# Kernel tuning notes

Hardware: AMD Instinct MI355X
Metric: run time of the kernel (lower is better)

## Reference

```python
import jax, jax.numpy as jnp
import numpy as np

B, S, H = 2, 2048, 2048
NH, HD = 32, 64            # num heads, head dim (H = NH*HD)
FFN = 8192
EPS = 1e-5


def _layernorm(x, g, b):
    mu = jnp.mean(x, axis=-1, keepdims=True)
    var = jnp.mean(jnp.square(x - mu), axis=-1, keepdims=True)
    return (x - mu) * jax.lax.rsqrt(var + EPS) * g + b


def setup_inputs() -> dict:
    key = jax.random.key(0)
    ks = jax.random.split(key, 8)
    s = lambda fan_in: 1.0 / np.sqrt(fan_in)
    return {
        "x": jax.random.normal(ks[0], (B, S, H), dtype=jnp.float32),
        "ln1_g": jnp.ones((H,), jnp.float32),
        "ln1_b": jnp.zeros((H,), jnp.float32),
        "w_qkv": jax.random.normal(ks[1], (H, 3 * H), jnp.float32) * s(H),
        "b_qkv": jnp.zeros((3 * H,), jnp.float32),
        "w_proj": jax.random.normal(ks[2], (H, H), jnp.float32) * s(H),
        "b_proj": jnp.zeros((H,), jnp.float32),
        "ln2_g": jnp.ones((H,), jnp.float32),
        "ln2_b": jnp.zeros((H,), jnp.float32),
        "w1": jax.random.normal(ks[3], (H, FFN), jnp.float32) * s(H),
        "b1": jnp.zeros((FFN,), jnp.float32),
        "w2": jax.random.normal(ks[4], (FFN, H), jnp.float32) * s(FFN),
        "b2": jnp.zeros((H,), jnp.float32),
    }


def reference(x, ln1_g, ln1_b, w_qkv, b_qkv, w_proj, b_proj,
              ln2_g, ln2_b, w1, b1, w2, b2):
    # Pre-LN attention block (dropout in eval mode -> identity)
    res = x
    h = _layernorm(x, ln1_g, ln1_b)
    qkv = h @ w_qkv + b_qkv                       # [B,S,3H]
    qkv = qkv.reshape(B, S, NH, 3 * HD)           # matches tf reshape+split on axis 3
    q, k, v = jnp.split(qkv, 3, axis=3)           # each [B,S,NH,HD]
    scores = jnp.einsum('bqhd,bkhd->bhqk', q, k) / jnp.sqrt(jnp.float32(HD))
    probs = jax.nn.softmax(scores, axis=-1)       # [B,NH,S,S]
    ctx = jnp.einsum('bhqk,bkhd->bqhd', probs, v).reshape(B, S, H)
    x = ctx @ w_proj + b_proj
    x = res + x
    # Pre-LN MLP block
    res = x
    h = _layernorm(x, ln2_g, ln2_b)
    h = jax.nn.gelu(h @ w1 + b1, approximate=True)
    h = h @ w2 + b2
    return h + res
```

## Files before the change

### kernel.cpp

```cpp
#include <hip/hip_runtime.h>
#include <hip/hip_bf16.h>
#include <math.h>


typedef __attribute__((ext_vector_type(8))) short bf16x8;
typedef __attribute__((ext_vector_type(4))) float f32x4;
typedef __attribute__((ext_vector_type(16))) float f32x16;

#define DEV __device__ __forceinline__

static constexpr int SEQ  = 2048;
static constexpr int HID  = 2048;
static constexpr int NHEAD = 32;
static constexpr int HDIM = 64;
static constexpr int NFFN = 8192;
static constexpr int NTOK = 2 * SEQ;
static constexpr int QKVW = 3 * HID;

#define QSCALE 0.1803368801111204f

#if defined(__has_builtin)
#if __has_builtin(__builtin_amdgcn_exp2f)
#define EXP2(x) __builtin_amdgcn_exp2f(x)
#endif
#endif
#ifndef EXP2
#define EXP2(x) exp2f(x)
#endif

#define VMCNT(n) asm volatile("s_waitcnt vmcnt(" #n ")" ::: "memory")
#define SB0()    __builtin_amdgcn_sched_barrier(0)

DEV ushort f2bf(float f) {
  unsigned u = __float_as_uint(f);
  return (ushort)((u + 0x7fffu + ((u >> 16) & 1u)) >> 16);
}

DEV void gload16(const void* g, void* l) {
  __builtin_amdgcn_global_load_lds(
      (const __attribute__((address_space(1))) unsigned int*)g,
      (__attribute__((address_space(3))) unsigned int*)l, 16, 0, 0);
}

__global__ __launch_bounds__(256) void tcvt_kernel(const float* __restrict__ in,
                                                   ushort* __restrict__ out,
                                                   int R, int C) {
  __shared__ ushort tile[64][72];
  const int tr = blockIdx.y * 64, tc = blockIdx.x * 64;
  const int t = threadIdx.x;
  const int rr = t >> 2, c4 = (t & 3) * 16;
  const float4* ip = (const float4*)(in + (size_t)(tr + rr) * C + tc + c4);
  float4 a0 = ip[0], a1 = ip[1], a2 = ip[2], a3 = ip[3];
  ushort* tp = &tile[rr][c4];
  tp[0]=f2bf(a0.x); tp[1]=f2bf(a0.y); tp[2]=f2bf(a0.z); tp[3]=f2bf(a0.w);
  tp[4]=f2bf(a1.x); tp[5]=f2bf(a1.y); tp[6]=f2bf(a1.z); tp[7]=f2bf(a1.w);
  tp[8]=f2bf(a2.x); tp[9]=f2bf(a2.y); tp[10]=f2bf(a2.z); tp[11]=f2bf(a2.w);
  tp[12]=f2bf(a3.x); tp[13]=f2bf(a3.y); tp[14]=f2bf(a3.z); tp[15]=f2bf(a3.w);
  __syncthreads();
  union { ushort u[8]; bf16x8 v; } p0, p1;
#pragma unroll
  for (int j = 0; j < 8; ++j) { p0.u[j] = tile[c4 + j][rr]; p1.u[j] = tile[c4 + 8 + j][rr]; }
  ushort* op = out + (size_t)(tc + rr) * R + tr + c4;
  *(bf16x8*)op = p0.v;
  *(bf16x8*)(op + 8) = p1.v;
}

__global__ __launch_bounds__(256) void ln_kernel(const float* __restrict__ x,
                                                 const float* __restrict__ g,
                                                 const float* __restrict__ bb,
                                                 ushort* __restrict__ out) {
  const int row = blockIdx.x, t = threadIdx.x;
  const float4* xv = (const float4*)(x + (size_t)row * HID);
  float4 a0 = xv[t * 2], a1 = xv[t * 2 + 1];
  float s  = a0.x + a0.y + a0.z + a0.w + a1.x + a1.y + a1.z + a1.w;
  float ss = a0.x*a0.x + a0.y*a0.y + a0.z*a0.z + a0.w*a0.w
           + a1.x*a1.x + a1.y*a1.y + a1.z*a1.z + a1.w*a1.w;
#pragma unroll
  for (int o = 32; o > 0; o >>= 1) { s += __shfl_down(s, o); ss += __shfl_down(ss, o); }
  __shared__ float red[8];
  const int w = t >> 6, l = t & 63;
  if (l == 0) { red[w] = s; red[4 + w] = ss; }
  __syncthreads();
  s  = red[0] + red[1] + red[2] + red[3];
  ss = red[4] + red[5] + red[6] + red[7];
  const float mu = s * (1.f / HID);
  const float rs = rsqrtf(ss * (1.f / HID) - mu * mu + 1e-5f);
  const float4* gv = (const float4*)g;
  const float4* bv = (const float4*)bb;
  float4 g0 = gv[t * 2], g1 = gv[t * 2 + 1], b0 = bv[t * 2], b1 = bv[t * 2 + 1];
  union { ushort u[8]; bf16x8 v; } p;
  p.u[0] = f2bf((a0.x - mu) * rs * g0.x + b0.x);
  p.u[1] = f2bf((a0.y - mu) * rs * g0.y + b0.y);
  p.u[2] = f2bf((a0.z - mu) * rs * g0.z + b0.z);
  p.u[3] = f2bf((a0.w - mu) * rs * g0.w + b0.w);
  p.u[4] = f2bf((a1.x - mu) * rs * g1.x + b1.x);
  p.u[5] = f2bf((a1.y - mu) * rs * g1.y + b1.y);
  p.u[6] = f2bf((a1.z - mu) * rs * g1.z + b1.z);
  p.u[7] = f2bf((a1.w - mu) * rs * g1.w + b1.w);
  *(bf16x8*)(out + (size_t)row * HID + t * 8) = p.v;
}

DEV void qkv_store(int row, int col, float v,
                   ushort* __restrict__ qpk, ushort* __restrict__ kpk,
                   ushort* __restrict__ vpk) {
  const int h = col / 192;
  const int c = col - h * 192;
  const int bh2 = (row >> 11) * 32 + h;
  const int t32 = (row >> 5) & 63;
  const int r5 = row & 31;
  if (c < 64) {
    const int s = c >> 4, hi2 = (c >> 3) & 1, j = c & 7;
    qpk[(((size_t)bh2 * 64 + t32) * 4 + s) * 512 + (hi2 * 32 + r5) * 8 + j] = f2bf(v * QSCALE);
  } else if (c < 128) {
    const int d = c - 64;
    const int s = d >> 4, hi2 = (d >> 3) & 1, j = d & 7;
    kpk[(((size_t)bh2 * 64 + t32) * 4 + s) * 512 + (hi2 * 32 + r5) * 8 + j] = f2bf(v);
  } else {
    const int d = c - 128;
    const int ks = r5 >> 4, hi2 = (r5 >> 3) & 1, j = r5 & 7;
    const int half = d >> 5, dl = d & 31;
    vpk[((((size_t)bh2 * 64 + t32) * 2 + ks) * 2 + half) * 512 + (hi2 * 32 + dl) * 8 + j] = f2bf(v);
  }
}

template <int BM, int EPI>
__global__ __launch_bounds__(512, 2) void gemm8p_kernel(
    const ushort* __restrict__ A, const ushort* __restrict__ BT,
    const float* __restrict__ bias, const float* __restrict__ res,
    void* __restrict__ outv,
    ushort* __restrict__ qpk, ushort* __restrict__ kpk, ushort* __restrict__ vpk,
    int M, int N, int K) {
  constexpr int MR = BM / 32;
  constexpr int MH = BM / 64;

  __shared__ ushort lds[2 * (BM * 64 + 256 * 64)];
  char* const a0p = (char*)lds;
  char* const b0p = a0p + BM * 128;
  char* const a1p = b0p + 32768;
  char* const b1p = a1p + BM * 128;

  const int t = threadIdx.x;
  const int w = t >> 6, l = t & 63;
  const int l16 = l & 15, lg = l >> 4;
  const int lr = l >> 3, lsl = l & 7;
  const int wm = w >> 2, wn = w & 3;
  const int l7 = l & 7;

  const int nwg = gridDim.x * gridDim.y;
  const int lin = blockIdx.y * gridDim.x + blockIdx.x;
  const int work = (lin & 7) * (nwg >> 3) + (lin >> 3);
  const int bn = work % gridDim.x, bm = work / gridDim.x;
  const int tm = bm * BM, tn = bn * 256;

  const int xk0 = (lg ^ l7) << 4;
  const int xk1 = ((lg + 4) ^ l7) << 4;
  const int aoff = (wm * (BM / 2) + l16) * 128;
  const int boff = (wn * 64 + l16) * 128;
  const char* rA0k0 = a0p + aoff + xk0;  const char* rA0k1 = a0p + aoff + xk1;
  const char* rA1k0 = a1p + aoff + xk0;  const char* rA1k1 = a1p + aoff + xk1;
  const char* rB0k0 = b0p + boff + xk0;  const char* rB0k1 = b0p + boff + xk1;
  const char* rB1k0 = b1p + boff + xk0;  const char* rB1k1 = b1p + boff + xk1;

  int rA00, rA01, rA10, rA11;
  if (BM == 256) {
    rA00 = 0 * 128 + 0 * 64 + w * 8 + lr;  rA01 = 1 * 128 + 0 * 64 + w * 8 + lr;
    rA10 = 0 * 128 + 1 * 64 + w * 8 + lr;  rA11 = 1 * 128 + 1 * 64 + w * 8 + lr;
  } else {
    const int ri = w * 8 + lr;
    rA00 = (ri >> 5) * 64 + 0 * 32 + (ri & 31);
    rA10 = (ri >> 5) * 64 + 1 * 32 + (ri & 31);
    rA01 = rA00; rA11 = rA10;
  }
  const int riB0 = w * 8 + lr, riB1 = 64 + w * 8 + lr;
  const int rB00 = (riB0 >> 5) * 64 + (riB0 & 31);
  const int rB01 = (riB1 >> 5) * 64 + (riB1 & 31);
  const int rB10 = (riB0 >> 5) * 64 + 32 + (riB0 & 31);
  const int rB11 = (riB1 >> 5) * 64 + 32 + (riB1 & 31);
  const int gcol = (lsl ^ lr) << 3;
  const ushort* pa00 = A + (size_t)(tm + rA00) * K + gcol;
  const ushort* pa01 = A + (size_t)(tm + rA01) * K + gcol;
  const ushort* pa10 = A + (size_t)(tm + rA10) * K + gcol;
  const ushort* pa11 = A + (size_t)(tm + rA11) * K + gcol;
  const ushort* pb00 = BT + (size_t)(tn + rB00) * K + gcol;
  const ushort* pb01 = BT + (size_t)(tn + rB01) * K + gcol;
  const ushort* pb10 = BT + (size_t)(tn + rB10) * K + gcol;
  const ushort* pb11 = BT + (size_t)(tn + rB11) * K + gcol;
  const int da00 = rA00 * 128 + lsl * 16, da01 = rA01 * 128 + lsl * 16;
  const int da10 = rA10 * 128 + lsl * 16, da11 = rA11 * 128 + lsl * 16;
  const int db00 = rB00 * 128 + lsl * 16, db01 = rB01 * 128 + lsl * 16;
  const int db10 = rB10 * 128 + lsl * 16, db11 = rB11 * 128 + lsl * 16;

  const f32x4 z4 = {0.f, 0.f, 0.f, 0.f};
  f32x4 acc[MR][4];
#pragma unroll
  for (int i = 0; i < MR; ++i)
#pragma unroll
    for (int j = 0; j < 4; ++j) acc[i][j] = z4;

  auto ktile = [&](const char* rAk0, const char* rAk1,
                   const char* rBk0, const char* rBk1,
                   char* NA, char* NB, int ktn, bool dost) {
    bf16x8 af[MH][2], bfr[2][2];
#pragma unroll
    for (int q = 0; q < 4; ++q) {
      const int mh = q >> 1, nh = q & 1;
      if ((q & 1) == 0) {
#pragma unroll
        for (int mi = 0; mi < MH; ++mi) {
          af[mi][0] = *(const bf16x8*)(rAk0 + mh * (BM / 4) * 128 + mi * 2048);
          af[mi][1] = *(const bf16x8*)(rAk1 + mh * (BM / 4) * 128 + mi * 2048);
        }
      }
#pragma unroll
      for (int ni = 0; ni < 2; ++ni) {
        bfr[ni][0] = *(const bf16x8*)(rBk0 + nh * 4096 + ni * 2048);
        bfr[ni][1] = *(const bf16x8*)(rBk1 + nh * 4096 + ni * 2048);
      }
      if (dost && q < 2) {
        if (q == 0) {
          gload16(pa00 + ktn, NA + da00);
          if (BM == 256) gload16(pa01 + ktn, NA + da01);
          gload16(pb00 + ktn, NB + db00);
          gload16(pb01 + ktn, NB + db01);
        } else {
          gload16(pa10 + ktn, NA + da10);
          if (BM == 256) gload16(pa11 + ktn, NA + da11);
          gload16(pb10 + ktn, NB + db10);
          gload16(pb11 + ktn, NB + db11);
        }
      }
      if (q == 0) {
        if (dost) { if (BM == 256) VMCNT(4); else VMCNT(3); }
        else VMCNT(0);
      }
      if (q == 3 && dost) { if (BM == 256) VMCNT(4); else VMCNT(3); }
      __builtin_amdgcn_s_barrier();
      asm volatile("s_waitcnt lgkmcnt(0)" ::: "memory");
      SB0();
      __builtin_amdgcn_s_setprio(1);
#pragma unroll
      for (int mi = 0; mi < MH; ++mi)
#pragma unroll
        for (int ni = 0; ni < 2; ++ni)
#pragma unroll
          for (int ks = 0; ks < 2; ++ks)
            acc[mh * MH + mi][nh * 2 + ni] = __builtin_amdgcn_mfma_f32_16x16x32_bf16(
                af[mi][ks], bfr[ni][ks], acc[mh * MH + mi][nh * 2 + ni], 0, 0, 0);
      __builtin_amdgcn_s_setprio(0);
    }
  };

  gload16(pa00, a0p + da00);
  if (BM == 256) gload16(pa01, a0p + da01);
  gload16(pb00, b0p + db00);
  gload16(pb01, b0p + db01);
  gload16(pa10, a0p + da10);
  if (BM == 256) gload16(pa11, a0p + da11);
  gload16(pb10, b0p + db10);
  gload16(pb11, b0p + db11);
  VMCNT(0);
  __builtin_amdgcn_s_barrier();

  const int nt = K >> 6;
  for (int it = 0; it < nt; it += 2) {
    ktile(rA0k0, rA0k1, rB0k0, rB0k1, a1p, b1p, (it + 1) << 6, true);
    ktile(rA1k0, rA1k1, rB1k0, rB1k1, a0p, b0p, (it + 2) << 6, (it + 2) < nt);
  }

  const int row0 = tm + wm * (BM / 2) + lg * 4;
  const int col0 = tn + wn * 64 + l16;
#pragma unroll
  for (int ni = 0; ni < 4; ++ni) {
    const int col = col0 + ni * 16;
    const float bvl = bias[col];
#pragma unroll
    for (int mi = 0; mi < MR; ++mi) {
#pragma unroll
      for (int r = 0; r < 4; ++r) {
        const int row = row0 + mi * 16 + r;
        float v = acc[mi][ni][r] + bvl;
        if (EPI == 1) {
          const size_t off = (size_t)row * N + col;
          ((float*)outv)[off] = v + res[off];
        } else if (EPI == 2) {
          const float u = 0.7978845608f * (v + 0.044715f * v * v * v);
          ((ushort*)outv)[(size_t)row * N + col] = f2bf(v / (1.f + __expf(-2.f * u)));
        } else if (EPI == 3) {
          qkv_store(row, col, v, qpk, kpk, vpk);
        } else {
          ((ushort*)outv)[(size_t)row * N + col] = f2bf(v);
        }
      }
    }
  }
}

__global__ __launch_bounds__(256) void attn_kernel(const ushort* __restrict__ qpk,
                                                   const ushort* __restrict__ kpk,
                                                   const ushort* __restrict__ vpk,
                                                   ushort* __restrict__ ctx) {
  const int lin = blockIdx.x + blockIdx.y * gridDim.x;
  const int work = (lin & 7) * 128 + (lin >> 3);
  const int qt = work & 15, bh = work >> 4;
  const int b = bh >> 5, h = bh & 31;
  const int t = threadIdx.x, w = t >> 6, l = t & 63;
  const int l32 = l & 31, hi = l >> 5;

  const ushort* qb = qpk + ((((size_t)bh * 64 + qt * 4 + w) * 4) * 64 + l) * 8;
  bf16x8 qf0 = *(const bf16x8*)(qb);
  bf16x8 qf1 = *(const bf16x8*)(qb + 512);
  bf16x8 qf2 = *(const bf16x8*)(qb + 1024);
  bf16x8 qf3 = *(const bf16x8*)(qb + 1536);

  const ushort* kbase = kpk + (size_t)bh * 131072 + l * 8;
  const ushort* vbase = vpk + (size_t)bh * 131072 + l * 8;

  f32x16 oacc0, oacc1;
#pragma unroll
  for (int r = 0; r < 16; ++r) { oacc0[r] = 0.f; oacc1[r] = 0.f; }
  float m = -1e30f, lsum = 0.f;
  const f32x16 z16 = {};

#define LOADK(k0, k1, k2, k3, kt) {                                           \
    const ushort* p_ = kbase + (size_t)(kt) * 2048;                           \
    k0 = *(const bf16x8*)(p_);        k1 = *(const bf16x8*)(p_ + 512);        \
    k2 = *(const bf16x8*)(p_ + 1024); k3 = *(const bf16x8*)(p_ + 1536); }
#define LOADV(v0, v1, v2, v3, kt) {                                           \
    const ushort* p_ = vbase + (size_t)(kt) * 2048;                           \
    v0 = *(const bf16x8*)(p_);        v1 = *(const bf16x8*)(p_ + 512);        \
    v2 = *(const bf16x8*)(p_ + 1024); v3 = *(const bf16x8*)(p_ + 1536); }

#define STEP(k0, k1, k2, k3, v0, v1, v2, v3) {                                \
    f32x16 s = __builtin_amdgcn_mfma_f32_32x32x16_bf16(k0, qf0, z16, 0, 0, 0);\
    s = __builtin_amdgcn_mfma_f32_32x32x16_bf16(k1, qf1, s, 0, 0, 0);         \
    s = __builtin_amdgcn_mfma_f32_32x32x16_bf16(k2, qf2, s, 0, 0, 0);         \
    s = __builtin_amdgcn_mfma_f32_32x32x16_bf16(k3, qf3, s, 0, 0, 0);         \
    float tm_ = s[0];                                                         \
    _Pragma("unroll") for (int r = 1; r < 16; ++r) tm_ = fmaxf(tm_, s[r]);    \
    tm_ = fmaxf(tm_, __shfl_xor(tm_, 32));                                    \
    if (!__all(tm_ - m <= 8.f)) {                                             \
      const float mn = fmaxf(m, tm_);                                         \
      const float sf = EXP2(m - mn);                                          \
      m = mn;                                                                 \
      lsum *= sf;                                                             \
      _Pragma("unroll") for (int r = 0; r < 16; ++r) {                        \
        const float f = __shfl(sf, (r & 3) + 8 * (r >> 2) + 4 * hi);          \
        oacc0[r] *= f; oacc1[r] *= f;                                         \
      }                                                                       \
    }                                                                         \
    float p[16];                                                              \
    _Pragma("unroll") for (int r = 0; r < 16; ++r) p[r] = EXP2(s[r] - m);     \
    float ls = 0.f;                                                           \
    _Pragma("unroll") for (int r = 0; r < 16; ++r) ls += p[r];                \
    lsum += ls;                                                               \
    unsigned pw[8];                                                           \
    _Pragma("unroll") for (int i = 0; i < 8; ++i)                             \
      asm("v_cvt_pk_bf16_f32 %0, %1, %2" : "=v"(pw[i]) : "v"(p[2*i]), "v"(p[2*i+1])); \
    unsigned a0 = pw[0], b0 = pw[2];                                          \
    asm("v_permlane32_swap_b32 %0, %1" : "+v"(a0), "+v"(b0));                 \
    unsigned a1 = pw[1], b1 = pw[3];                                          \
    asm("v_permlane32_swap_b32 %0, %1" : "+v"(a1), "+v"(b1));                 \
    unsigned a2 = pw[4], b2 = pw[6];                                          \
    asm("v_permlane32_swap_b32 %0, %1" : "+v"(a2), "+v"(b2));                 \
    unsigned a3 = pw[5], b3 = pw[7];                                          \
    asm("v_permlane32_swap_b32 %0, %1" : "+v"(a3), "+v"(b3));                 \
    union { unsigned uw[4]; bf16x8 v; } pa0, pa1;                             \
    pa0.uw[0] = a0; pa0.uw[1] = a1; pa0.uw[2] = b0; pa0.uw[3] = b1;           \
    pa1.uw[0] = a2; pa1.uw[1] = a3; pa1.uw[2] = b2; pa1.uw[3] = b3;           \
    oacc0 = __builtin_amdgcn_mfma_f32_32x32x16_bf16(pa0.v, v0, oacc0, 0, 0, 0);\
    oacc1 = __builtin_amdgcn_mfma_f32_32x32x16_bf16(pa0.v, v1, oacc1, 0, 0, 0);\
    oacc0 = __builtin_amdgcn_mfma_f32_32x32x16_bf16(pa1.v, v2, oacc0, 0, 0, 0);\
    oacc1 = __builtin_amdgcn_mfma_f32_32x32x16_bf16(pa1.v, v3, oacc1, 0, 0, 0);}

  bf16x8 ka0, ka1, ka2, ka3, kc0, kc1, kc2, kc3;
  LOADK(ka0, ka1, ka2, ka3, 0);
  for (int kt = 0; kt < 64; kt += 2) {
    bf16x8 va0, va1, va2, va3;
    LOADV(va0, va1, va2, va3, kt);
    LOADK(kc0, kc1, kc2, kc3, kt + 1);
    STEP(ka0, ka1, ka2, ka3, va0, va1, va2, va3);
    LOADV(va0, va1, va2, va3, kt + 1);
    if (kt + 2 < 64) LOADK(ka0, ka1, ka2, ka3, kt + 2);
    STEP(kc0, kc1, kc2, kc3, va0, va1, va2, va3);
  }
#undef LOADK
#undef LOADV
#undef STEP

  const float lf = lsum + __shfl_xor(lsum, 32);
  const float linv = 1.f / lf;
#pragma unroll
  for (int r = 0; r < 16; ++r) {
    const int qr = (r & 3) + 8 * (r >> 2);
    const float fac = __shfl(linv, qr + 4 * hi);
    const int row = qt * 128 + w * 32 + qr + 4 * hi;
    const size_t base = ((size_t)(b * SEQ + row)) * HID + h * 64 + l32;
    ctx[base]      = f2bf(oacc0[r] * fac);
    ctx[base + 32] = f2bf(oacc1[r] * fac);
  }
}

extern "C" void kernel_launch(void* const* d_in, const int* in_sizes, int n_in,
                              void* d_out, int out_size, void* d_ws, size_t ws_size,
                              hipStream_t stream) {
  const float* x      = (const float*)d_in[0];
  const float* ln1g   = (const float*)d_in[1];
  const float* ln1b   = (const float*)d_in[2];
  const float* w_qkv  = (const float*)d_in[3];
  const float* b_qkv  = (const float*)d_in[4];
  const float* w_proj = (const float*)d_in[5];
  const float* b_proj = (const float*)d_in[6];
  const float* ln2g   = (const float*)d_in[7];
  const float* ln2b   = (const float*)d_in[8];
  const float* w1     = (const float*)d_in[9];
  const float* b1     = (const float*)d_in[10];
  const float* w2     = (const float*)d_in[11];
  const float* b2     = (const float*)d_in[12];

  char* ws = (char*)d_ws;
  ushort* wqkvT  = (ushort*)(ws + 0);
  ushort* wprojT = (ushort*)(ws + 25165824);
  ushort* w1T    = (ushort*)(ws + 33554432);
  ushort* w2T    = (ushort*)(ws + 67108864);
  ushort* hbuf   = (ushort*)(ws + 100663296);
  ushort* qpk    = (ushort*)(ws + 117440512);
  ushort* kpk    = (ushort*)(ws + 134217728);
  ushort* vpk    = (ushort*)(ws + 150994944);
  ushort* ctxb   = (ushort*)(ws + 167772160);
  ushort* gelu   = (ushort*)(ws + 117440512);
  float*  x2     = (float*)(ws + 184549376);

  tcvt_kernel<<<dim3(96, 32),  256, 0, stream>>>(w_qkv,  wqkvT, 2048, 6144);
  tcvt_kernel<<<dim3(32, 32),  256, 0, stream>>>(w_proj, wprojT, 2048, 2048);
  tcvt_kernel<<<dim3(128, 32), 256, 0, stream>>>(w1,     w1T,   2048, 8192);
  tcvt_kernel<<<dim3(32, 128), 256, 0, stream>>>(w2,     w2T,   8192, 2048);

  ln_kernel<<<NTOK, 256, 0, stream>>>(x, ln1g, ln1b, hbuf);
  gemm8p_kernel<128, 3><<<dim3(24, 32), 512, 0, stream>>>(
      hbuf, wqkvT, b_qkv, nullptr, nullptr, qpk, kpk, vpk, NTOK, QKVW, HID);
  attn_kernel<<<dim3(16, 2 * NHEAD), 256, 0, stream>>>(qpk, kpk, vpk, ctxb);
  gemm8p_kernel<128, 1><<<dim3(8, 32), 512, 0, stream>>>(
      ctxb, wprojT, b_proj, x, x2, nullptr, nullptr, nullptr, NTOK, HID, HID);
  ln_kernel<<<NTOK, 256, 0, stream>>>(x2, ln2g, ln2b, hbuf);
  gemm8p_kernel<256, 2><<<dim3(32, 16), 512, 0, stream>>>(
      hbuf, w1T, b1, nullptr, gelu, nullptr, nullptr, nullptr, NTOK, NFFN, HID);
  gemm8p_kernel<128, 1><<<dim3(8, 32), 512, 0, stream>>>(
      gelu, w2T, b2, x2, (float*)d_out, nullptr, nullptr, nullptr, NTOK, HID, NFFN);
}
```

Baseline: 633.4 us.

## Add ping-pong pipelined 256x256 GEMM kernel for the FFN up-projection

Adds a new 256x256-tile bf16 GEMM kernel that splits each tile into four 128-wide halves in LDS. It interleaves per-half global-to-LDS loads with MFMA sub-blocks using barriers, explicit waitcnts and setprio, and uses an XOR-swizzled layout. It replaces the previous gemm8p<256,2> launch for the w1 GEMM with fused GELU, aiming to overlap memory traffic with matrix math more tightly. The many barriers and the 128KB LDS footprint cost occupancy and scheduling flexibility, in exchange for deeper software pipelining.

```diff
diff --git a/kernel.cpp b/kernel.cpp
--- a/kernel.cpp
+++ b/kernel.cpp
@@ -287,6 +287,176 @@
           ((ushort*)outv)[(size_t)row * N + col] = f2bf(v / (1.f + __expf(-2.f * u)));
         } else if (EPI == 3) {
           qkv_store(row, col, v, qpk, kpk, vpk);
+        } else {
+          ((ushort*)outv)[(size_t)row * N + col] = f2bf(v);
+        }
+      }
+    }
+  }
+}
+
+template <int EPI>
+__global__ __launch_bounds__(512, 2) void gemm256p_kernel(
+    const ushort* __restrict__ A, const ushort* __restrict__ BT,
+    const float* __restrict__ bias, const float* __restrict__ res,
+    void* __restrict__ outv, int M, int N, int K) {
+  __shared__ ushort lds[65536];
+  char* const L = (char*)lds;
+
+  const int t = threadIdx.x;
+  const int w = t >> 6, l = t & 63;
+  const int l16 = l & 15, lg = l >> 4, lr = l >> 3, lsl = l & 7, l7 = l & 7;
+  const int wm = w >> 2, wn = w & 3;
+
+  const int nwg = gridDim.x * gridDim.y;
+  const int lin = blockIdx.y * gridDim.x + blockIdx.x;
+  const int work = (lin & 7) * (nwg >> 3) + (lin >> 3);
+  const int bn = work % gridDim.x, bm = work / gridDim.x;
+  const int tm = bm * 256, tn = bn * 256;
+
+  char* Ab[2][2]; char* Bb[2][2];
+#pragma unroll
+  for (int par = 0; par < 2; ++par)
+#pragma unroll
+    for (int h = 0; h < 2; ++h) {
+      Ab[par][h] = L + (par * 2 + h) * 16384;
+      Bb[par][h] = L + 65536 + (par * 2 + h) * 16384;
+    }
+
+  const int xk0 = (lg ^ l7) << 4, xk1 = ((4 + lg) ^ l7) << 4;
+  const char* pA[2][2]; const char* pB[2][2];
+#pragma unroll
+  for (int par = 0; par < 2; ++par) {
+    const char* ab = Ab[par][wm] + l16 * 128;
+    const char* bb = Bb[par][wn >> 1] + ((wn & 1) * 64 + l16) * 128;
+    pA[par][0] = ab + xk0; pA[par][1] = ab + xk1;
+    pB[par][0] = bb + xk0; pB[par][1] = bb + xk1;
+  }
+
+  const int gcol = (lsl ^ lr) << 3;
+  const ushort* gA[2][2]; const ushort* gB[2][2];
+  int dst[2];
+#pragma unroll
+  for (int s = 0; s < 2; ++s) {
+    const int r = s * 64 + w * 8 + lr;
+    dst[s] = r * 128 + lsl * 16;
+#pragma unroll
+    for (int h = 0; h < 2; ++h) {
+      gA[h][s] = A + (size_t)(tm + h * 128 + r) * K + gcol;
+      gB[h][s] = BT + (size_t)(tn + h * 128 + r) * K + gcol;
+    }
+  }
+
+  f32x4 acc[8][4];
+  const f32x4 z4 = {0.f, 0.f, 0.f, 0.f};
+#pragma unroll
+  for (int i = 0; i < 8; ++i)
+#pragma unroll
+    for (int j = 0; j < 4; ++j) acc[i][j] = z4;
+
+  auto rdA = [&](int par, int mh, bf16x8 (&af)[4][2]) {
+#pragma unroll
+    for (int mi = 0; mi < 4; ++mi) {
+      af[mi][0] = *(const bf16x8*)(pA[par][0] + mh * 8192 + mi * 2048);
+      af[mi][1] = *(const bf16x8*)(pA[par][1] + mh * 8192 + mi * 2048);
+    }
+  };
+  auto rdB = [&](int par, int nh, bf16x8 (&bf)[2][2]) {
+#pragma unroll
+    for (int ni = 0; ni < 2; ++ni) {
+      bf[ni][0] = *(const bf16x8*)(pB[par][0] + nh * 4096 + ni * 2048);
+      bf[ni][1] = *(const bf16x8*)(pB[par][1] + nh * 4096 + ni * 2048);
+    }
+  };
+  auto mf16 = [&](int mh, int nh, bf16x8 (&af)[4][2], bf16x8 (&bf)[2][2]) {
+    __builtin_amdgcn_s_setprio(1);
+#pragma unroll
+    for (int mi = 0; mi < 4; ++mi)
+#pragma unroll
+      for (int ni = 0; ni < 2; ++ni)
+#pragma unroll
+        for (int ks = 0; ks < 2; ++ks)
+          acc[mh * 4 + mi][nh * 2 + ni] = __builtin_amdgcn_mfma_f32_16x16x32_bf16(
+              af[mi][ks], bf[ni][ks], acc[mh * 4 + mi][nh * 2 + ni], 0, 0, 0);
+    __builtin_amdgcn_s_setprio(0);
+  };
+#define BAR() __builtin_amdgcn_s_barrier()
+#define LGKM0() do { asm volatile("s_waitcnt lgkmcnt(0)" ::: "memory"); SB0(); } while (0)
+
+#pragma unroll
+  for (int h = 0; h < 2; ++h)
+#pragma unroll
+    for (int s = 0; s < 2; ++s) gload16(gA[h][s], Ab[0][h] + dst[s]);
+#pragma unroll
+  for (int h = 0; h < 2; ++h)
+#pragma unroll
+    for (int s = 0; s < 2; ++s) gload16(gB[h][s], Bb[0][h] + dst[s]);
+#pragma unroll
+  for (int h = 0; h < 2; ++h)
+#pragma unroll
+    for (int s = 0; s < 2; ++s) gload16(gB[h][s] + 64, Bb[1][h] + dst[s]);
+  VMCNT(4);
+  BAR();
+
+  const int nt = K >> 6;
+  for (int it = 0; it < nt; it += 2) {
+    const int k1 = (it + 1) << 6, k2 = (it + 2) << 6, k3 = (it + 3) << 6;
+    const bool s2 = (it + 2) < nt;
+    bf16x8 af[4][2], b0[2][2], b1[2][2];
+    rdA(0, 0, af); rdB(0, 0, b0);
+    gload16(gA[0][0] + k1, Ab[1][0] + dst[0]);
+    gload16(gA[0][1] + k1, Ab[1][0] + dst[1]);
+    BAR(); LGKM0(); mf16(0, 0, af, b0); BAR();
+    rdB(0, 1, b1);
+    gload16(gA[1][0] + k1, Ab[1][1] + dst[0]);
+    gload16(gA[1][1] + k1, Ab[1][1] + dst[1]);
+    BAR(); LGKM0(); mf16(0, 1, af, b1); BAR();
+    rdA(0, 1, af);
+    if (s2) { gload16(gB[0][0] + k2, Bb[0][0] + dst[0]);
+              gload16(gB[0][1] + k2, Bb[0][0] + dst[1]); }
+    BAR(); LGKM0(); mf16(1, 1, af, b1); BAR();
+    if (s2) { gload16(gB[1][0] + k2, Bb[0][1] + dst[0]);
+              gload16(gB[1][1] + k2, Bb[0][1] + dst[1]); }
+    BAR(); LGKM0(); mf16(1, 0, af, b0);
+    if (s2) VMCNT(4); else VMCNT(0);
+    BAR();
+    rdA(1, 0, af); rdB(1, 0, b0);
+    if (s2) { gload16(gA[0][0] + k2, Ab[0][0] + dst[0]);
+              gload16(gA[0][1] + k2, Ab[0][0] + dst[1]); }
+    BAR(); LGKM0(); mf16(0, 0, af, b0); BAR();
+    rdB(1, 1, b1);
+    if (s2) { gload16(gA[1][0] + k2, Ab[0][1] + dst[0]);
+              gload16(gA[1][1] + k2, Ab[0][1] + dst[1]); }
+    BAR(); LGKM0(); mf16(0, 1, af, b1); BAR();
+    rdA(1, 1, af);
+    if (s2) { gload16(gB[0][0] + k3, Bb[1][0] + dst[0]);
+              gload16(gB[0][1] + k3, Bb[1][0] + dst[1]); }
+    BAR(); LGKM0(); mf16(1, 1, af, b1); BAR();
+    if (s2) { gload16(gB[1][0] + k3, Bb[1][1] + dst[0]);
+              gload16(gB[1][1] + k3, Bb[1][1] + dst[1]); }
+    BAR(); LGKM0(); mf16(1, 0, af, b0);
+    if (s2) VMCNT(4); else VMCNT(0);
+    BAR();
+  }
+#undef BAR
+#undef LGKM0
+
+#pragma unroll
+  for (int nf = 0; nf < 4; ++nf) {
+    const int col = tn + wn * 64 + nf * 16 + l16;
+    const float bvl = bias[col];
+#pragma unroll
+    for (int mf = 0; mf < 8; ++mf) {
+#pragma unroll
+      for (int r = 0; r < 4; ++r) {
+        const int row = tm + wm * 128 + mf * 16 + lg * 4 + r;
+        float v = acc[mf][nf][r] + bvl;
+        if (EPI == 1) {
+          const size_t off = (size_t)row * N + col;
+          ((float*)outv)[off] = v + res[off];
+        } else if (EPI == 2) {
+          const float u = 0.7978845608f * (v + 0.044715f * v * v * v);
+          ((ushort*)outv)[(size_t)row * N + col] = f2bf(v / (1.f + __expf(-2.f * u)));
         } else {
           ((ushort*)outv)[(size_t)row * N + col] = f2bf(v);
         }
@@ -442,8 +612,8 @@
   gemm8p_kernel<128, 1><<<dim3(8, 32), 512, 0, stream>>>(
       ctxb, wprojT, b_proj, x, x2, nullptr, nullptr, nullptr, NTOK, HID, HID);
   ln_kernel<<<NTOK, 256, 0, stream>>>(x2, ln2g, ln2b, hbuf);
-  gemm8p_kernel<256, 2><<<dim3(32, 16), 512, 0, stream>>>(
-      hbuf, w1T, b1, nullptr, gelu, nullptr, nullptr, nullptr, NTOK, NFFN, HID);
+  gemm256p_kernel<2><<<dim3(32, 16), 512, 0, stream>>>(
+      hbuf, w1T, b1, nullptr, gelu, NTOK, NFFN, HID);
   gemm8p_kernel<128, 1><<<dim3(8, 32), 512, 0, stream>>>(
       gelu, w2T, b2, x2, (float*)d_out, nullptr, nullptr, nullptr, NTOK, HID, NFFN);
 }
```

Result: slower. 1.001 ms (+58.1%).

## Add triple-buffered 128x256 GEMM kernel with XCD-aware tile swizzle

Applied to the files above, without the earlier changes.

Introduces a new GEMM kernel, gemm3b, that keeps three LDS stages so global loads run two K-tiles ahead of the MFMA work. It remaps workgroup IDs so neighbouring tiles are grouped across the 8 dispatch partitions, and raises wave priority around the MFMA block. The QKV, output-projection and FFN-down GEMMs switch to this kernel to hide memory latency better than the previous double-buffered one. In exchange it uses more LDS per block (about 144KB), which may limit occupancy, and it adds a sizeable macro-based code path.

```diff
diff --git a/kernel.cpp b/kernel.cpp
--- a/kernel.cpp
+++ b/kernel.cpp
@@ -275,6 +275,143 @@
     const float bvl = bias[col];
 #pragma unroll
     for (int mi = 0; mi < MR; ++mi) {
+#pragma unroll
+      for (int r = 0; r < 4; ++r) {
+        const int row = row0 + mi * 16 + r;
+        float v = acc[mi][ni][r] + bvl;
+        if (EPI == 1) {
+          const size_t off = (size_t)row * N + col;
+          ((float*)outv)[off] = v + res[off];
+        } else if (EPI == 2) {
+          const float u = 0.7978845608f * (v + 0.044715f * v * v * v);
+          ((ushort*)outv)[(size_t)row * N + col] = f2bf(v / (1.f + __expf(-2.f * u)));
+        } else if (EPI == 3) {
+          qkv_store(row, col, v, qpk, kpk, vpk);
+        } else {
+          ((ushort*)outv)[(size_t)row * N + col] = f2bf(v);
+        }
+      }
+    }
+  }
+}
+
+#define G3BODY(CB, SB)                                                         \
+  {                                                                            \
+    const bool s2_ = (tt + 2) < nt;                                            \
+    if (s2_) {                                                                 \
+      const int k2_ = (tt + 2) << 6;                                           \
+      gload16(ga0 + k2_, Ab##SB + da0); gload16(ga1 + k2_, Ab##SB + da1);      \
+      gload16(gb0 + k2_, Bb##SB + db0); gload16(gb1 + k2_, Bb##SB + db1);      \
+      gload16(gb2 + k2_, Bb##SB + db2); gload16(gb3 + k2_, Bb##SB + db3);      \
+    }                                                                          \
+    bf16x8 af_[4][2], bf_[4][2];                                               \
+    _Pragma("unroll") for (int mf = 0; mf < 4; ++mf) {                         \
+      af_[mf][0] = *(const bf16x8*)(pA##CB##0 + mf * 2048);                    \
+      af_[mf][1] = *(const bf16x8*)(pA##CB##1 + mf * 2048);                    \
+    }                                                                          \
+    _Pragma("unroll") for (int nf = 0; nf < 4; ++nf) {                         \
+      bf_[nf][0] = *(const bf16x8*)(pB##CB##0 + nf * 2048);                    \
+      bf_[nf][1] = *(const bf16x8*)(pB##CB##1 + nf * 2048);                    \
+    }                                                                          \
+    __builtin_amdgcn_s_setprio(1);                                             \
+    _Pragma("unroll") for (int mf = 0; mf < 4; ++mf)                           \
+      _Pragma("unroll") for (int nf = 0; nf < 4; ++nf)                         \
+        _Pragma("unroll") for (int ks = 0; ks < 2; ++ks)                       \
+          acc[mf][nf] = __builtin_amdgcn_mfma_f32_16x16x32_bf16(               \
+              af_[mf][ks], bf_[nf][ks], acc[mf][nf], 0, 0, 0);                 \
+    __builtin_amdgcn_s_setprio(0);                                             \
+    asm volatile("s_waitcnt lgkmcnt(0)" ::: "memory");                         \
+    if (s2_) { VMCNT(6); }                                                     \
+    else if (tt + 1 < nt) { VMCNT(0); }                                        \
+    __builtin_amdgcn_s_barrier();                                              \
+  }
+
+template <int EPI>
+__global__ __launch_bounds__(512, 2) void gemm3b_kernel(
+    const ushort* __restrict__ A, const ushort* __restrict__ BT,
+    const float* __restrict__ bias, const float* __restrict__ res,
+    void* __restrict__ outv,
+    ushort* __restrict__ qpk, ushort* __restrict__ kpk, ushort* __restrict__ vpk,
+    int M, int N, int K) {
+  __shared__ ushort lds[73728];
+  char* const L = (char*)lds;
+  char* const Ab0 = L;             char* const Bb0 = L + 16384;
+  char* const Ab1 = L + 49152;     char* const Bb1 = Ab1 + 16384;
+  char* const Ab2 = L + 98304;     char* const Bb2 = Ab2 + 16384;
+
+  const int t = threadIdx.x;
+  const int w = t >> 6, l = t & 63;
+  const int l16 = l & 15, lg = l >> 4, lr = l >> 3, lsl = l & 7, l7 = l & 7;
+  const int wm = w >> 2, wn = w & 3;
+
+  const int nwg = gridDim.x * gridDim.y;
+  const int lin = blockIdx.y * gridDim.x + blockIdx.x;
+  const int work = (lin & 7) * (nwg >> 3) + (lin >> 3);
+  const int bn = work % gridDim.x, bm = work / gridDim.x;
+  const int tm = bm * 128, tn = bn * 256;
+
+  const int xk0 = (lg ^ l7) << 4, xk1 = ((4 + lg) ^ l7) << 4;
+  const int aoff = (wm * 64 + l16) * 128;
+  const int boff = (wn * 64 + l16) * 128;
+  const char* pA00 = Ab0 + aoff + xk0;  const char* pA01 = Ab0 + aoff + xk1;
+  const char* pA10 = Ab1 + aoff + xk0;  const char* pA11 = Ab1 + aoff + xk1;
+  const char* pA20 = Ab2 + aoff + xk0;  const char* pA21 = Ab2 + aoff + xk1;
+  const char* pB00 = Bb0 + boff + xk0;  const char* pB01 = Bb0 + boff + xk1;
+  const char* pB10 = Bb1 + boff + xk0;  const char* pB11 = Bb1 + boff + xk1;
+  const char* pB20 = Bb2 + boff + xk0;  const char* pB21 = Bb2 + boff + xk1;
+
+  const int ri = w * 8 + lr;
+  const int rA0 = (ri >> 5) * 64 + (ri & 31);
+  const int rA1 = rA0 + 32;
+  const int ri2 = 64 + ri;
+  const int rB0 = rA0;
+  const int rB1 = (ri2 >> 5) * 64 + (ri2 & 31);
+  const int rB2 = rB0 + 32;
+  const int rB3 = rB1 + 32;
+  const int gcol = (lsl ^ lr) << 3;
+  const ushort* ga0 = A + (size_t)(tm + rA0) * K + gcol;
+  const ushort* ga1 = A + (size_t)(tm + rA1) * K + gcol;
+  const ushort* gb0 = BT + (size_t)(tn + rB0) * K + gcol;
+  const ushort* gb1 = BT + (size_t)(tn + rB1) * K + gcol;
+  const ushort* gb2 = BT + (size_t)(tn + rB2) * K + gcol;
+  const ushort* gb3 = BT + (size_t)(tn + rB3) * K + gcol;
+  const int da0 = rA0 * 128 + lsl * 16, da1 = rA1 * 128 + lsl * 16;
+  const int db0 = rB0 * 128 + lsl * 16, db1 = rB1 * 128 + lsl * 16;
+  const int db2 = rB2 * 128 + lsl * 16, db3 = rB3 * 128 + lsl * 16;
+
+  const f32x4 z4 = {0.f, 0.f, 0.f, 0.f};
+  f32x4 acc[4][4];
+#pragma unroll
+  for (int i = 0; i < 4; ++i)
+#pragma unroll
+    for (int j = 0; j < 4; ++j) acc[i][j] = z4;
+
+  const int nt = K >> 6;
+
+  gload16(ga0, Ab0 + da0); gload16(ga1, Ab0 + da1);
+  gload16(gb0, Bb0 + db0); gload16(gb1, Bb0 + db1);
+  gload16(gb2, Bb0 + db2); gload16(gb3, Bb0 + db3);
+  gload16(ga0 + 64, Ab1 + da0); gload16(ga1 + 64, Ab1 + da1);
+  gload16(gb0 + 64, Bb1 + db0); gload16(gb1 + 64, Bb1 + db1);
+  gload16(gb2 + 64, Bb1 + db2); gload16(gb3 + 64, Bb1 + db3);
+  VMCNT(6);
+  __builtin_amdgcn_s_barrier();
+
+  int tt = 0;
+  while (true) {
+    G3BODY(0, 2); ++tt; if (tt >= nt) break;
+    G3BODY(1, 0); ++tt; if (tt >= nt) break;
+    G3BODY(2, 1); ++tt; if (tt >= nt) break;
+  }
+
+  const int row0 = tm + wm * 64 + lg * 4;
+  const int col0 = tn + wn * 64 + l16;
+#pragma unroll
+  for (int ni = 0; ni < 4; ++ni) {
+    const int col = col0 + ni * 16;
+    const float bvl = bias[col];
+#pragma unroll
+    for (int mi = 0; mi < 4; ++mi) {
 #pragma unroll
       for (int r = 0; r < 4; ++r) {
         const int row = row0 + mi * 16 + r;
@@ -436,14 +573,14 @@
   tcvt_kernel<<<dim3(32, 128), 256, 0, stream>>>(w2,     w2T,   8192, 2048);
 
   ln_kernel<<<NTOK, 256, 0, stream>>>(x, ln1g, ln1b, hbuf);
-  gemm8p_kernel<128, 3><<<dim3(24, 32), 512, 0, stream>>>(
+  gemm3b_kernel<3><<<dim3(24, 32), 512, 0, stream>>>(
       hbuf, wqkvT, b_qkv, nullptr, nullptr, qpk, kpk, vpk, NTOK, QKVW, HID);
   attn_kernel<<<dim3(16, 2 * NHEAD), 256, 0, stream>>>(qpk, kpk, vpk, ctxb);
-  gemm8p_kernel<128, 1><<<dim3(8, 32), 512, 0, stream>>>(
+  gemm3b_kernel<1><<<dim3(8, 32), 512, 0, stream>>>(
       ctxb, wprojT, b_proj, x, x2, nullptr, nullptr, nullptr, NTOK, HID, HID);
   ln_kernel<<<NTOK, 256, 0, stream>>>(x2, ln2g, ln2b, hbuf);
   gemm8p_kernel<256, 2><<<dim3(32, 16), 512, 0, stream>>>(
       hbuf, w1T, b1, nullptr, gelu, nullptr, nullptr, nullptr, NTOK, NFFN, HID);
-  gemm8p_kernel<128, 1><<<dim3(8, 32), 512, 0, stream>>>(
+  gemm3b_kernel<1><<<dim3(8, 32), 512, 0, stream>>>(
       gelu, w2T, b2, x2, (float*)d_out, nullptr, nullptr, nullptr, NTOK, HID, NFFN);
 }
```

After: 622.2 us. About the same (-1.8%).
